# Performance work log

Hardware: AMD Instinct MI355X
Metric: run time of the kernel (lower is better)

The kernel has to match this reference:

```python
import jax, jax.numpy as jnp
import numpy as np

TEMPERATURE = 0.5
N, D = 8192, 256
N_CLASSES = 64


def setup_inputs() -> dict:
    key = jax.random.key(0)
    k1, k2 = jax.random.split(key)
    emb = jax.random.normal(k1, (N, D), dtype=jnp.float32)
    # original module expects normalized embeddings
    emb = emb / jnp.linalg.norm(emb, axis=-1, keepdims=True)
    labels = jax.random.randint(k2, (N,), 0, N_CLASSES, dtype=jnp.int64)
    return {"embeddings": emb, "epitope_labels": labels}


def reference(embeddings, epitope_labels):
    n = embeddings.shape[0]
    # [N, N] pairwise similarities
    sim = jnp.matmul(embeddings, embeddings.T) / TEMPERATURE
    eye = jnp.eye(n, dtype=bool)
    labels_eq = epitope_labels[None, :] == epitope_labels[:, None]
    mask_pos = labels_eq & ~eye  # positives exclude self
    # row-max subtraction (detached, matches torch .detach())
    sim_max = jax.lax.stop_gradient(jnp.max(sim, axis=1, keepdims=True))
    shifted = sim - sim_max
    exp_sim = jnp.exp(shifted)
    # denominator excludes the diagonal (self-similarity)
    denom = jnp.sum(jnp.where(eye, 0.0, exp_sim), axis=1)  # [N]
    # per-pair loss: -log(exp_sim_ij / denom_i) = -(shifted_ij - log denom_i)
    per_pair = -(shifted - jnp.log(denom)[:, None])
    # mean over positive pairs (equivalent to masked_select + repeat_interleave + mean)
    n_pos = jnp.sum(mask_pos)
    loss = jnp.sum(jnp.where(mask_pos, per_pair, 0.0)) / n_pos
    return loss
```

## Files before the change

kernel.cpp:

```cpp
#include <hip/hip_runtime.h>
#include <hip/hip_bf16.h>

#define N 8192
#define D 256

typedef __attribute__((ext_vector_type(8))) short bf16x8;
typedef __attribute__((ext_vector_type(4))) float f32x4;

#define BM 128
#define BN 64
#define COLS_PER_BLK 512
#define NT (COLS_PER_BLK / BN)
#define ROWBLKS (N / BM)
#define COLBLKS (N / COLS_PER_BLK)

__device__ inline unsigned short f2bf(float x) {
    __hip_bfloat16 h = __float2bfloat16(x);
    return *reinterpret_cast<unsigned short*>(&h);
}

__global__ void convert_kernel(const float4* __restrict__ E4, ushort4* __restrict__ Ebf4,
                               float* __restrict__ Z, float* __restrict__ P, float* __restrict__ C) {
    int i = blockIdx.x * blockDim.x + threadIdx.x;
    int n4 = (N * D) / 4;
    if (i < n4) {
        float4 v = E4[i];
        ushort4 o;
        o.x = f2bf(v.x); o.y = f2bf(v.y); o.z = f2bf(v.z); o.w = f2bf(v.w);
        Ebf4[i] = o;
    }
    if (i < N) { Z[i] = 0.0f; P[i] = 0.0f; C[i] = 0.0f; }
}

__global__ __launch_bounds__(256)
void sim_kernel(const __hip_bfloat16* __restrict__ Ebf,
                const int* __restrict__ labels,
                float* __restrict__ Z, float* __restrict__ P, float* __restrict__ C) {
    __shared__ unsigned char Bsh[BN * 512];
    __shared__ int Lcol[COLS_PER_BLK];

    const int tid  = threadIdx.x;
    const int lane = tid & 63;
    const int wid  = tid >> 6;
    const int blk  = blockIdx.x;
    const int r0   = (blk >> 4) * BM;
    const int c0   = (blk & 15) * COLS_PER_BLK;

    for (int t = tid; t < COLS_PER_BLK; t += 256) Lcol[t] = labels[c0 + t];

    const char* ebase = (const char*)Ebf;

    bf16x8 a[2][8];
#pragma unroll
    for (int rg = 0; rg < 2; ++rg) {
        int row = r0 + wid * 32 + rg * 16 + (lane & 15);
        const char* rp = ebase + (size_t)row * (D * 2) + ((lane >> 4) * 16);
#pragma unroll
        for (int kg = 0; kg < 8; ++kg)
            a[rg][kg] = *reinterpret_cast<const bf16x8*>(rp + kg * 64);
    }

    int labi[2][4];
#pragma unroll
    for (int rg = 0; rg < 2; ++rg)
#pragma unroll
        for (int r = 0; r < 4; ++r)
            labi[rg][r] = labels[r0 + wid * 32 + rg * 16 + (lane >> 4) * 4 + r];

    float zacc[2][4] = {{0}}, pacc[2][4] = {{0}}, cacc[2][4] = {{0}};

    for (int ct = 0; ct < NT; ++ct) {
        __syncthreads();
#pragma unroll
        for (int m = 0; m < 8; ++m) {
            unsigned obase = m * 4096 + wid * 1024;
            unsigned o     = obase + lane * 16;
            unsigned row   = o >> 9;
            unsigned inner = (o & 511) ^ ((row & 7) << 4);
            const char* src = ebase + (size_t)(c0 + ct * 64 + row) * (D * 2) + inner;
            __builtin_amdgcn_global_load_lds(
                (const __attribute__((address_space(1))) void*)src,
                (__attribute__((address_space(3))) void*)(Bsh + obase), 16, 0, 0);
        }
        __syncthreads();

        f32x4 acc[2][4];
#pragma unroll
        for (int rg = 0; rg < 2; ++rg)
#pragma unroll
            for (int cg = 0; cg < 4; ++cg) acc[rg][cg] = (f32x4){0.f, 0.f, 0.f, 0.f};

#pragma unroll
        for (int cg = 0; cg < 4; ++cg) {
            int col = cg * 16 + (lane & 15);
            unsigned rowbase = (unsigned)col * 512;
            unsigned ib = (lane >> 4) * 16;
#pragma unroll
            for (int kg = 0; kg < 8; ++kg) {
                unsigned inner = (ib + kg * 64) ^ ((col & 7) << 4);
                bf16x8 b = *reinterpret_cast<const bf16x8*>(Bsh + rowbase + inner);
                acc[0][cg] = __builtin_amdgcn_mfma_f32_16x16x32_bf16(a[0][kg], b, acc[0][cg], 0, 0, 0);
                acc[1][cg] = __builtin_amdgcn_mfma_f32_16x16x32_bf16(a[1][kg], b, acc[1][cg], 0, 0, 0);
            }
        }

#pragma unroll
        for (int rg = 0; rg < 2; ++rg)
#pragma unroll
            for (int cg = 0; cg < 4; ++cg) {
                int jloc = ct * 64 + cg * 16 + (lane & 15);
                int j    = c0 + jloc;
                int labj = Lcol[jloc];
#pragma unroll
                for (int r = 0; r < 4; ++r) {
                    int i = r0 + wid * 32 + rg * 16 + (lane >> 4) * 4 + r;
                    float s = 2.0f * acc[rg][cg][r];
                    float e = __expf(s - 2.0f);
                    bool diag = (i == j);
                    bool pos  = (labi[rg][r] == labj) && !diag;
                    zacc[rg][r] += diag ? 0.0f : e;
                    pacc[rg][r] += pos ? s : 0.0f;
                    cacc[rg][r] += pos ? 1.0f : 0.0f;
                }
            }
    }

#pragma unroll
    for (int rg = 0; rg < 2; ++rg)
#pragma unroll
        for (int r = 0; r < 4; ++r) {
            float z = zacc[rg][r], p = pacc[rg][r], c = cacc[rg][r];
#pragma unroll
            for (int m = 8; m >= 1; m >>= 1) {
                z += __shfl_xor(z, m, 64);
                p += __shfl_xor(p, m, 64);
                c += __shfl_xor(c, m, 64);
            }
            if ((lane & 15) == 0) {
                int i = r0 + wid * 32 + rg * 16 + (lane >> 4) * 4 + r;
                atomicAdd(&Z[i], z);
                atomicAdd(&P[i], p);
                atomicAdd(&C[i], c);
            }
        }
}

__global__ void finalize_kernel(const float* __restrict__ Z, const float* __restrict__ P,
                                const float* __restrict__ C, float* __restrict__ out) {
    __shared__ float snum[256], sden[256];
    float num = 0.0f, den = 0.0f;
    for (int i = threadIdx.x; i < N; i += 256) {
        float c = C[i];
        num += c * (2.0f + logf(Z[i])) - P[i];
        den += c;
    }
    snum[threadIdx.x] = num; sden[threadIdx.x] = den;
    __syncthreads();
    for (int s = 128; s > 0; s >>= 1) {
        if (threadIdx.x < s) {
            snum[threadIdx.x] += snum[threadIdx.x + s];
            sden[threadIdx.x] += sden[threadIdx.x + s];
        }
        __syncthreads();
    }
    if (threadIdx.x == 0) out[0] = snum[0] / sden[0];
}

extern "C" void kernel_launch(void* const* d_in, const int* in_sizes, int n_in,
                              void* d_out, int out_size, void* d_ws, size_t ws_size,
                              hipStream_t stream) {
    const float* emb   = (const float*)d_in[0];
    const int* labels  = (const int*)d_in[1];
    float* out = (float*)d_out;

    char* ws = (char*)d_ws;
    __hip_bfloat16* Ebf = (__hip_bfloat16*)ws;
    float* Z = (float*)(ws + (size_t)N * D * 2);
    float* P = Z + N;
    float* C = P + N;

    convert_kernel<<<(N * D / 4 + 255) / 256, 256, 0, stream>>>(
        (const float4*)emb, (ushort4*)Ebf, Z, P, C);
    sim_kernel<<<ROWBLKS * COLBLKS, 256, 0, stream>>>(Ebf, labels, Z, P, C);
    finalize_kernel<<<1, 256, 0, stream>>>(Z, P, C, out);
}
```

Before: 126.3 us.

## Strip diagonal/count logic from epilogue, use exp2 and histogram counts

```diff
diff --git a/kernel.cpp b/kernel.cpp
--- a/kernel.cpp
+++ b/kernel.cpp
@@ -14,13 +14,25 @@
 #define ROWBLKS (N / BM)
 #define COLBLKS (N / COLS_PER_BLK)
 
+#define K1 2.8853900817779268f
+#define K2 (-2.8853900817779268f)
+
 __device__ inline unsigned short f2bf(float x) {
     __hip_bfloat16 h = __float2bfloat16(x);
     return *reinterpret_cast<unsigned short*>(&h);
 }
 
+__device__ inline float fast_exp2(float t) {
+#if __has_builtin(__builtin_amdgcn_exp2f)
+    return __builtin_amdgcn_exp2f(t);
+#else
+    return __expf(t * 0.69314718056f);
+#endif
+}
+
 __global__ void convert_kernel(const float4* __restrict__ E4, ushort4* __restrict__ Ebf4,
-                               float* __restrict__ Z, float* __restrict__ P, float* __restrict__ C) {
+                               float* __restrict__ Z, float* __restrict__ P,
+                               float* __restrict__ nd) {
     int i = blockIdx.x * blockDim.x + threadIdx.x;
     int n4 = (N * D) / 4;
     if (i < n4) {
@@ -29,13 +41,14 @@
         o.x = f2bf(v.x); o.y = f2bf(v.y); o.z = f2bf(v.z); o.w = f2bf(v.w);
         Ebf4[i] = o;
     }
-    if (i < N) { Z[i] = 0.0f; P[i] = 0.0f; C[i] = 0.0f; }
+    if (i < N) { Z[i] = 0.0f; P[i] = 0.0f; }
+    if (i < 2) nd[i] = 0.0f;
 }
 
 __global__ __launch_bounds__(256)
 void sim_kernel(const __hip_bfloat16* __restrict__ Ebf,
                 const int* __restrict__ labels,
-                float* __restrict__ Z, float* __restrict__ P, float* __restrict__ C) {
+                float* __restrict__ Z, float* __restrict__ P) {
     __shared__ unsigned char Bsh[BN * 512];
     __shared__ int Lcol[COLS_PER_BLK];
 
@@ -67,20 +80,30 @@
         for (int r = 0; r < 4; ++r)
             labi[rg][r] = labels[r0 + wid * 32 + rg * 16 + (lane >> 4) * 4 + r];
 
-    float zacc[2][4] = {{0}}, pacc[2][4] = {{0}}, cacc[2][4] = {{0}};
+    unsigned rbase[4];
+#pragma unroll
+    for (int cg = 0; cg < 4; ++cg) {
+        unsigned col = cg * 16 + (lane & 15);
+        unsigned seg = lane >> 4;
+        rbase[cg] = (col * 64 + seg * 16) ^ (((col >> 1) & 3) << 4);
+    }
+
+    float zacc[2][4] = {{0}}, pacc[2][4] = {{0}};
 
     for (int ct = 0; ct < NT; ++ct) {
         __syncthreads();
 #pragma unroll
         for (int m = 0; m < 8; ++m) {
-            unsigned obase = m * 4096 + wid * 1024;
-            unsigned o     = obase + lane * 16;
-            unsigned row   = o >> 9;
-            unsigned inner = (o & 511) ^ ((row & 7) << 4);
-            const char* src = ebase + (size_t)(c0 + ct * 64 + row) * (D * 2) + inner;
+            int c = wid * 8 + m;
+            int kg = c >> 2, colblk = c & 3;
+            unsigned dbase = kg * 4096 + colblk * 1024;
+            int colLocal = colblk * 16 + (lane >> 2);
+            int seg_src  = (lane & 3) ^ ((colLocal >> 1) & 3);
+            const char* src = ebase + (size_t)(c0 + ct * 64 + colLocal) * 512
+                            + kg * 64 + seg_src * 16;
             __builtin_amdgcn_global_load_lds(
                 (const __attribute__((address_space(1))) void*)src,
-                (__attribute__((address_space(3))) void*)(Bsh + obase), 16, 0, 0);
+                (__attribute__((address_space(3))) void*)(Bsh + dbase), 16, 0, 0);
         }
         __syncthreads();
 
@@ -92,95 +115,92 @@
 
 #pragma unroll
         for (int cg = 0; cg < 4; ++cg) {
-            int col = cg * 16 + (lane & 15);
-            unsigned rowbase = (unsigned)col * 512;
-            unsigned ib = (lane >> 4) * 16;
 #pragma unroll
             for (int kg = 0; kg < 8; ++kg) {
-                unsigned inner = (ib + kg * 64) ^ ((col & 7) << 4);
-                bf16x8 b = *reinterpret_cast<const bf16x8*>(Bsh + rowbase + inner);
+                bf16x8 b = *reinterpret_cast<const bf16x8*>(Bsh + rbase[cg] + kg * 4096);
                 acc[0][cg] = __builtin_amdgcn_mfma_f32_16x16x32_bf16(a[0][kg], b, acc[0][cg], 0, 0, 0);
                 acc[1][cg] = __builtin_amdgcn_mfma_f32_16x16x32_bf16(a[1][kg], b, acc[1][cg], 0, 0, 0);
             }
         }
 
 #pragma unroll
-        for (int rg = 0; rg < 2; ++rg)
-#pragma unroll
-            for (int cg = 0; cg < 4; ++cg) {
-                int jloc = ct * 64 + cg * 16 + (lane & 15);
-                int j    = c0 + jloc;
-                int labj = Lcol[jloc];
+        for (int cg = 0; cg < 4; ++cg) {
+            int labj = Lcol[ct * 64 + cg * 16 + (lane & 15)];
+#pragma unroll
+            for (int rg = 0; rg < 2; ++rg)
 #pragma unroll
                 for (int r = 0; r < 4; ++r) {
-                    int i = r0 + wid * 32 + rg * 16 + (lane >> 4) * 4 + r;
-                    float s = 2.0f * acc[rg][cg][r];
-                    float e = __expf(s - 2.0f);
-                    bool diag = (i == j);
-                    bool pos  = (labi[rg][r] == labj) && !diag;
-                    zacc[rg][r] += diag ? 0.0f : e;
-                    pacc[rg][r] += pos ? s : 0.0f;
-                    cacc[rg][r] += pos ? 1.0f : 0.0f;
+                    float d = acc[rg][cg][r];
+                    zacc[rg][r] += fast_exp2(__builtin_fmaf(d, K1, K2));
+                    pacc[rg][r] += (labi[rg][r] == labj) ? d : 0.0f;
                 }
-            }
+        }
     }
 
 #pragma unroll
     for (int rg = 0; rg < 2; ++rg)
 #pragma unroll
         for (int r = 0; r < 4; ++r) {
-            float z = zacc[rg][r], p = pacc[rg][r], c = cacc[rg][r];
-#pragma unroll
-            for (int m = 8; m >= 1; m >>= 1) {
+            float z = zacc[rg][r], p = pacc[rg][r];
+#pragma unroll
+            for (int m = 1; m <= 8; m <<= 1) {
                 z += __shfl_xor(z, m, 64);
                 p += __shfl_xor(p, m, 64);
-                c += __shfl_xor(c, m, 64);
             }
             if ((lane & 15) == 0) {
                 int i = r0 + wid * 32 + rg * 16 + (lane >> 4) * 4 + r;
                 atomicAdd(&Z[i], z);
                 atomicAdd(&P[i], p);
-                atomicAdd(&C[i], c);
             }
         }
 }
 
 __global__ void finalize_kernel(const float* __restrict__ Z, const float* __restrict__ P,
-                                const float* __restrict__ C, float* __restrict__ out) {
+                                const int* __restrict__ labels, float* __restrict__ nd) {
+    __shared__ int hist[64];
     __shared__ float snum[256], sden[256];
-    float num = 0.0f, den = 0.0f;
-    for (int i = threadIdx.x; i < N; i += 256) {
-        float c = C[i];
-        num += c * (2.0f + logf(Z[i])) - P[i];
-        den += c;
-    }
-    snum[threadIdx.x] = num; sden[threadIdx.x] = den;
+    int t = threadIdx.x;
+    if (t < 64) hist[t] = 0;
+    __syncthreads();
+    for (int i = t; i < N; i += 256) atomicAdd(&hist[labels[i]], 1);
+    __syncthreads();
+
+    int i = blockIdx.x * 256 + t;
+    float z = Z[i] - 1.0f;
+    float p = 2.0f * (P[i] - 1.0f);
+    float c = (float)(hist[labels[i]] - 1);
+    float num = c * (2.0f + __logf(z)) - p;
+    float den = c;
+
+    snum[t] = num; sden[t] = den;
     __syncthreads();
     for (int s = 128; s > 0; s >>= 1) {
-        if (threadIdx.x < s) {
-            snum[threadIdx.x] += snum[threadIdx.x + s];
-            sden[threadIdx.x] += sden[threadIdx.x + s];
-        }
+        if (t < s) { snum[t] += snum[t + s]; sden[t] += sden[t + s]; }
         __syncthreads();
     }
-    if (threadIdx.x == 0) out[0] = snum[0] / sden[0];
+    if (t == 0) { atomicAdd(&nd[0], snum[0]); atomicAdd(&nd[1], sden[0]); }
+}
+
+__global__ void div_kernel(const float* __restrict__ nd, float* __restrict__ out) {
+    out[0] = nd[0] / nd[1];
 }
 
 extern "C" void kernel_launch(void* const* d_in, const int* in_sizes, int n_in,
                               void* d_out, int out_size, void* d_ws, size_t ws_size,
                               hipStream_t stream) {
-    const float* emb   = (const float*)d_in[0];
-    const int* labels  = (const int*)d_in[1];
+    const float* emb  = (const float*)d_in[0];
+    const int* labels = (const int*)d_in[1];
     float* out = (float*)d_out;
 
     char* ws = (char*)d_ws;
     __hip_bfloat16* Ebf = (__hip_bfloat16*)ws;
-    float* Z = (float*)(ws + (size_t)N * D * 2);
-    float* P = Z + N;
-    float* C = P + N;
+    float* Z  = (float*)(ws + (size_t)N * D * 2);
+    float* P  = Z + N;
+    float* nd = P + N;
 
     convert_kernel<<<(N * D / 4 + 255) / 256, 256, 0, stream>>>(
-        (const float4*)emb, (ushort4*)Ebf, Z, P, C);
-    sim_kernel<<<ROWBLKS * COLBLKS, 256, 0, stream>>>(Ebf, labels, Z, P, C);
-    finalize_kernel<<<1, 256, 0, stream>>>(Z, P, C, out);
-}
+        (const float4*)emb, (ushort4*)Ebf, Z, P, nd);
+    sim_kernel<<<ROWBLKS * COLBLKS, 256, 0, stream>>>(Ebf, labels, Z, P);
+    finalize_kernel<<<N / 256, 256, 0, stream>>>(Z, P, labels, nd);
+    div_kernel<<<1, 1, 0, stream>>>(nd, out);
+}
```

Result: faster. 113.2 us (-10.3%).
